# Optimization experiments

Measured on AMD Instinct MI355X. Metric: run time of the kernel, lower is better.

The kernel has to match this reference:

```python
import jax, jax.numpy as jnp
import numpy as np

TOP_K = 8
SCORE_FUNC = "sigmoid"
ROUTE_NORM = True
ROUTE_SCALE = 2.5


def setup_inputs() -> dict:
    key = jax.random.key(0)
    k1, k2, k3 = jax.random.split(key, 3)
    B, S, H, E = 4, 4096, 2048, 64
    hidden_states = jax.random.normal(k1, (B, S, H), dtype=jnp.float32)
    # nn.Linear default init scale ~ 1/sqrt(H); exact distribution irrelevant for correctness
    gate_w = jax.random.normal(k2, (E, H), dtype=jnp.float32) * (1.0 / np.sqrt(H))
    expert_bias = jax.random.normal(k3, (E,), dtype=jnp.float32) * 0.1
    return {"hidden_states": hidden_states, "expert_bias": expert_bias, "gate_w": gate_w}


def reference(hidden_states, expert_bias, gate_w):
    B, S, H = hidden_states.shape
    x = hidden_states.reshape(-1, H)  # [T, H]
    logits = jnp.einsum("th,eh->te", x, gate_w)  # [T, E]
    if SCORE_FUNC == "sigmoid":
        scores = jax.nn.sigmoid(logits.astype(jnp.float32))
    else:
        scores = jax.nn.softmax(logits.astype(jnp.float32), axis=-1)
    if expert_bias is not None:
        _, selected_experts = jax.lax.top_k(scores + expert_bias[None, :], TOP_K)
        top_scores = jnp.take_along_axis(scores, selected_experts, axis=1)
    else:
        top_scores, selected_experts = jax.lax.top_k(scores, TOP_K)
    if SCORE_FUNC == "sigmoid" and ROUTE_NORM:
        denom = jnp.sum(top_scores, axis=-1, keepdims=True) + 1e-20
        top_scores = top_scores / denom
    top_scores = top_scores * ROUTE_SCALE
    return top_scores, selected_experts
```

## Files before the change

### kernel.cpp

```cpp
#include <hip/hip_runtime.h>
#include <math.h>

#define T_TOTAL 16384
#define HDIM    2048
#define NEXP    64

typedef unsigned short ushort_t;
using bf16x8 = __attribute__((ext_vector_type(8))) short;
using f32x4  = __attribute__((ext_vector_type(4))) float;

__device__ __forceinline__ unsigned cvtpk_bf16(float a, float b) {
    unsigned r;
    asm("v_cvt_pk_bf16_f32 %0, %1, %2" : "=v"(r) : "v"(a), "v"(b));
    return r;
}

__device__ __forceinline__ void split8(const float4 a, const float4 b,
                                       bf16x8& h, bf16x8& m, bf16x8& l) {
    const float f[8] = {a.x, a.y, a.z, a.w, b.x, b.y, b.z, b.w};
    union { unsigned u[4]; bf16x8 v; } H, M, L;
#pragma unroll
    for (int d = 0; d < 4; ++d) {
        const float f0 = f[2*d], f1 = f[2*d+1];
        const unsigned ph = cvtpk_bf16(f0, f1);
        const float r0 = f0 - __uint_as_float(ph << 16);
        const float r1 = f1 - __uint_as_float(ph & 0xFFFF0000u);
        const unsigned pm = cvtpk_bf16(r0, r1);
        const float s0 = r0 - __uint_as_float(pm << 16);
        const float s1 = r1 - __uint_as_float(pm & 0xFFFF0000u);
        H.u[d] = ph;
        M.u[d] = pm;
        L.u[d] = cvtpk_bf16(s0, s1);
    }
    h = H.v; m = M.v; l = L.v;
}

__device__ __forceinline__ void load_lds16(const void* g, void* lds) {
    __builtin_amdgcn_global_load_lds(
        (const __attribute__((address_space(1))) unsigned int*)g,
        (__attribute__((address_space(3))) unsigned int*)lds, 16, 0, 0);
}

__device__ __forceinline__ int xswz(int row) {
    return ((row & 7) << 1) | ((row >> 3) & 1);
}

__global__ __launch_bounds__(256)
void convert_w_kernel(const float* __restrict__ w, ushort_t* __restrict__ wt)
{
    const int idx = blockIdx.x * 256 + threadIdx.x;
    const int e   = idx >> 8;
    const int c8  = idx & 255;
    const int kc  = c8 >> 3;
    const int c   = c8 & 7;

    const float* src = w + (size_t)e * HDIM + kc * 64 + c * 8;
    const float4 v0 = *(const float4*)(src);
    const float4 v1 = *(const float4*)(src + 4);
    bf16x8 H, M, L;
    split8(v0, v1, H, M, L);

    const int slot = c ^ (e & 7);
    bf16x8* base = (bf16x8*)wt;
    base[((size_t)(kc * 3 + 0) * 64 + e) * 8 + slot] = H;
    base[((size_t)(kc * 3 + 1) * 64 + e) * 8 + slot] = M;
    base[((size_t)(kc * 3 + 2) * 64 + e) * 8 + slot] = L;
}

__global__ __launch_bounds__(256, 2)
void router_fused(const float* __restrict__ x,
                  const ushort_t* __restrict__ wt,
                  const float* __restrict__ bias,
                  float* __restrict__ out_scores,
                  float* __restrict__ out_idx)
{
    __shared__ __align__(16) float    Xs[2][32 * 64];
    __shared__ __align__(16) ushort_t Ws[2][3 * 64 * 64];

    const int tid  = threadIdx.x;
    const int wv   = tid >> 6;
    const int lane = tid & 63;
    const int t0   = blockIdx.x * 32;
    const int a    = wv >> 1;
    const int b    = wv & 1;
    const int lr   = lane & 15;
    const int lg   = lane >> 4;

    const float bv = bias[lane];

    const int xrow0 = wv * 8 + (lane >> 4);
    const int xrow1 = xrow0 + 4;
    const float* xsrc0 = x + (size_t)(t0 + xrow0) * HDIM + ((lane & 15) ^ xswz(xrow0)) * 4;
    const float* xsrc1 = x + (size_t)(t0 + xrow1) * HDIM + ((lane & 15) ^ xswz(xrow1)) * 4;

    const ushort_t* wsrc = wt + (size_t)(wv * 6) * 512 + lane * 8;

    f32x4 acc[8];
#pragma unroll
    for (int i = 0; i < 8; ++i) {
        f32x4 z = {0.0f, 0.0f, 0.0f, 0.0f};
        acc[i] = z;
    }

    const int rowX = a * 16 + lr;
    const int swzX = xswz(rowX);

    auto stage = [&](int kc, int bi) {
        const int ko = kc * 64;
        load_lds16(xsrc0 + ko, &Xs[bi][(wv * 2 + 0) * 256]);
        load_lds16(xsrc1 + ko, &Xs[bi][(wv * 2 + 1) * 256]);
        const ushort_t* wn = wsrc + (size_t)kc * 12288;
#pragma unroll
        for (int q = 0; q < 6; ++q)
            load_lds16(wn + q * 512, &Ws[bi][(wv * 6 + q) * 512]);
    };

#define COMPUTE(BI, PAR) do {                                                 \
    const float*  rb  = &Xs[BI][rowX * 64];                                   \
    const bf16x8* wbp = (const bf16x8*)&Ws[BI][0];                            \
    _Pragma("unroll")                                                         \
    for (int ks = 0; ks < 2; ++ks) {                                          \
        const int g0 = ks * 8 + lg * 2;                                       \
        const float4 c0 = *(const float4*)(rb + ((g0       ^ swzX) * 4));     \
        const float4 c1 = *(const float4*)(rb + (((g0 + 1) ^ swzX) * 4));     \
        bf16x8 Ah, Am, Al;                                                    \
        split8(c0, c1, Ah, Am, Al);                                           \
        _Pragma("unroll")                                                     \
        for (int n = 0; n < 2; ++n) {                                         \
            const int e    = b * 32 + n * 16 + lr;                            \
            const int slot = (ks * 4 + lg) ^ (e & 7);                         \
            const bf16x8 Bh = wbp[(0 * 64 + e) * 8 + slot];                   \
            const bf16x8 Bm = wbp[(1 * 64 + e) * 8 + slot];                   \
            const bf16x8 Bl = wbp[(2 * 64 + e) * 8 + slot];                   \
            f32x4 t = acc[(PAR) * 4 + ks * 2 + n];                            \
            t = __builtin_amdgcn_mfma_f32_16x16x32_bf16(Ah, Bh, t, 0, 0, 0);  \
            t = __builtin_amdgcn_mfma_f32_16x16x32_bf16(Am, Bh, t, 0, 0, 0);  \
            t = __builtin_amdgcn_mfma_f32_16x16x32_bf16(Ah, Bm, t, 0, 0, 0);  \
            t = __builtin_amdgcn_mfma_f32_16x16x32_bf16(Am, Bm, t, 0, 0, 0);  \
            t = __builtin_amdgcn_mfma_f32_16x16x32_bf16(Al, Bh, t, 0, 0, 0);  \
            t = __builtin_amdgcn_mfma_f32_16x16x32_bf16(Ah, Bl, t, 0, 0, 0);  \
            t = __builtin_amdgcn_mfma_f32_16x16x32_bf16(Al, Bm, t, 0, 0, 0);  \
            t = __builtin_amdgcn_mfma_f32_16x16x32_bf16(Am, Bl, t, 0, 0, 0);  \
            acc[(PAR) * 4 + ks * 2 + n] = t;                                  \
        }                                                                     \
    }                                                                         \
} while (0)

    stage(0, 0);
    __syncthreads();

#pragma unroll 1
    for (int j = 0; j < 16; ++j) {
        const int kc0 = j * 2;
        stage(kc0 + 1, 1);
        COMPUTE(0, 0);
        __syncthreads();
        if (kc0 + 2 < 32) stage(kc0 + 2, 0);
        COMPUTE(1, 1);
        __syncthreads();
    }
#undef COMPUTE

    float* ov = &Xs[0][0];
#pragma unroll
    for (int n = 0; n < 2; ++n) {
        const f32x4 s = (acc[0 * 4 + 0 * 2 + n] + acc[0 * 4 + 1 * 2 + n])
                      + (acc[1 * 4 + 0 * 2 + n] + acc[1 * 4 + 1 * 2 + n]);
#pragma unroll
        for (int r = 0; r < 4; ++r) {
            const int t = a * 16 + lg * 4 + r;
            const int e = b * 32 + n * 16 + lr;
            ov[t * 64 + e] = s[r];
        }
    }
    __syncthreads();

#pragma unroll 1
    for (int i = 0; i < 8; ++i) {
        const int t = wv * 8 + i;
        const float logit = ov[t * 64 + lane];

        const float score = 1.0f / (1.0f + expf(-logit));
        float key = score + bv;

        float myscore = 0.0f;
        int   myidx   = 0;
        float denom   = 0.0f;

#pragma unroll
        for (int r = 0; r < 8; ++r) {
            float bk = key;
#pragma unroll
            for (int off = 32; off > 0; off >>= 1)
                bk = fmaxf(bk, __shfl_xor(bk, off));
            const unsigned long long msk = __ballot(key == bk);
            const int bi = __ffsll((long long)msk) - 1;
            const float wsc = __shfl(score, bi);
            denom += wsc;
            if (lane == r)  { myscore = wsc; myidx = bi; }
            if (lane == bi) key = -__builtin_inff();
        }

        const float factor = 2.5f / (denom + 1e-20f);
        if (lane < 8) {
            out_scores[(size_t)(t0 + t) * 8 + lane] = myscore * factor;
            out_idx  [(size_t)(t0 + t) * 8 + lane] = (float)myidx;
        }
    }
}

__global__ void router_gemm_naive(const float* __restrict__ x,
                                  const float* __restrict__ w,
                                  float* __restrict__ partial)
{
    const int t = blockIdx.x;
    const int e = threadIdx.x;
    const float* xp = x + (size_t)t * HDIM;
    const float* wp = w + (size_t)e * HDIM;
    float s = 0.0f;
    for (int k = 0; k < HDIM; ++k) s = fmaf(xp[k], wp[k], s);
    partial[(size_t)t * NEXP + e] = s;
}

__global__ __launch_bounds__(256)
void router_topk_naive(const float* __restrict__ partial,
                       const float* __restrict__ bias,
                       float* __restrict__ out_scores,
                       float* __restrict__ out_idx)
{
    const int token = blockIdx.x * 4 + (threadIdx.x >> 6);
    const int lane  = threadIdx.x & 63;
    const float logit = partial[(size_t)token * NEXP + lane];
    const float score = 1.0f / (1.0f + expf(-logit));
    float key = score + bias[lane];
    float myscore = 0.0f; int myidx = 0; float denom = 0.0f;
#pragma unroll
    for (int r = 0; r < 8; ++r) {
        float bk = key;
#pragma unroll
        for (int off = 32; off > 0; off >>= 1)
            bk = fmaxf(bk, __shfl_xor(bk, off));
        const unsigned long long msk = __ballot(key == bk);
        const int bi = __ffsll((long long)msk) - 1;
        const float wsc = __shfl(score, bi);
        denom += wsc;
        if (lane == r)  { myscore = wsc; myidx = bi; }
        if (lane == bi) key = -__builtin_inff();
    }
    const float factor = 2.5f / (denom + 1e-20f);
    if (lane < 8) {
        out_scores[(size_t)token * 8 + lane] = myscore * factor;
        out_idx  [(size_t)token * 8 + lane] = (float)myidx;
    }
}

extern "C" void kernel_launch(void* const* d_in, const int* in_sizes, int n_in,
                              void* d_out, int out_size, void* d_ws, size_t ws_size,
                              hipStream_t stream)
{
    const float* x    = (const float*)d_in[0];
    const float* bias = (const float*)d_in[1];
    const float* w    = (const float*)d_in[2];

    float* out = (float*)d_out;

    const size_t wtBytes = (size_t)3 * NEXP * HDIM * sizeof(ushort_t);

    if (ws_size >= wtBytes) {
        ushort_t* wt = (ushort_t*)d_ws;
        convert_w_kernel<<<dim3(64), dim3(256), 0, stream>>>(w, wt);
        router_fused<<<dim3(T_TOTAL / 32), dim3(256), 0, stream>>>(
            x, wt, bias, out, out + (size_t)T_TOTAL * 8);
    } else {
        float* partial = (float*)d_ws;
        router_gemm_naive<<<dim3(T_TOTAL), dim3(64), 0, stream>>>(x, w, partial);
        router_topk_naive<<<dim3(T_TOTAL / 4), dim3(256), 0, stream>>>(
            partial, bias, out, out + (size_t)T_TOTAL * 8);
    }
}
```

Before: 229.3 us.

## Read pre-packed weight fragments directly from global, drop weight LDS staging

The weight-conversion kernel now writes bf16 hi/mid/lo fragments in the exact per-lane MFMA register order, so the router kernel loads B operands straight from global/L2 instead of staging the 48KB of weights per block through LDS. The block grows to 512 threads (8 waves, each owning a 16x16 output tile), and LDS shrinks to just the X tile. This cuts LDS traffic and footprint to allow higher occupancy, but B loads now hit the cache each iteration with latency not hidden by double-buffering.

Result: no change. 232.0 us (+1.2%).

```diff
diff --git a/kernel.cpp b/kernel.cpp
--- a/kernel.cpp
+++ b/kernel.cpp
@@ -48,56 +48,56 @@
 __global__ __launch_bounds__(256)
 void convert_w_kernel(const float* __restrict__ w, ushort_t* __restrict__ wt)
 {
-    const int idx = blockIdx.x * 256 + threadIdx.x;
-    const int e   = idx >> 8;
-    const int c8  = idx & 255;
-    const int kc  = c8 >> 3;
-    const int c   = c8 & 7;
-
-    const float* src = w + (size_t)e * HDIM + kc * 64 + c * 8;
+    const int f  = blockIdx.x * 256 + threadIdx.x;
+    const int kc = f >> 9;
+    const int ks = (f >> 8) & 1;
+    const int nt = (f >> 6) & 3;
+    const int l  = f & 63;
+    const int e  = nt * 16 + (l & 15);
+    const int k  = kc * 64 + ks * 32 + (l >> 4) * 8;
+
+    const float* src = w + (size_t)e * HDIM + k;
     const float4 v0 = *(const float4*)(src);
     const float4 v1 = *(const float4*)(src + 4);
     bf16x8 H, M, L;
     split8(v0, v1, H, M, L);
 
-    const int slot = c ^ (e & 7);
-    bf16x8* base = (bf16x8*)wt;
-    base[((size_t)(kc * 3 + 0) * 64 + e) * 8 + slot] = H;
-    base[((size_t)(kc * 3 + 1) * 64 + e) * 8 + slot] = M;
-    base[((size_t)(kc * 3 + 2) * 64 + e) * 8 + slot] = L;
-}
-
-__global__ __launch_bounds__(256, 2)
+    bf16x8* out = (bf16x8*)wt;
+    const int base = (f >> 6) * 3;
+    out[(size_t)(base + 0) * 64 + l] = H;
+    out[(size_t)(base + 1) * 64 + l] = M;
+    out[(size_t)(base + 2) * 64 + l] = L;
+}
+
+__global__ __launch_bounds__(512, 4)
 void router_fused(const float* __restrict__ x,
                   const ushort_t* __restrict__ wt,
                   const float* __restrict__ bias,
                   float* __restrict__ out_scores,
                   float* __restrict__ out_idx)
 {
-    __shared__ __align__(16) float    Xs[2][32 * 64];
-    __shared__ __align__(16) ushort_t Ws[2][3 * 64 * 64];
+    __shared__ __align__(16) float Xs[2][32 * 64];
 
     const int tid  = threadIdx.x;
     const int wv   = tid >> 6;
     const int lane = tid & 63;
     const int t0   = blockIdx.x * 32;
-    const int a    = wv >> 1;
-    const int b    = wv & 1;
+    const int a    = wv >> 2;
+    const int b    = wv & 3;
     const int lr   = lane & 15;
     const int lg   = lane >> 4;
 
     const float bv = bias[lane];
 
-    const int xrow0 = wv * 8 + (lane >> 4);
-    const int xrow1 = xrow0 + 4;
-    const float* xsrc0 = x + (size_t)(t0 + xrow0) * HDIM + ((lane & 15) ^ xswz(xrow0)) * 4;
-    const float* xsrc1 = x + (size_t)(t0 + xrow1) * HDIM + ((lane & 15) ^ xswz(xrow1)) * 4;
-
-    const ushort_t* wsrc = wt + (size_t)(wv * 6) * 512 + lane * 8;
-
-    f32x4 acc[8];
-#pragma unroll
-    for (int i = 0; i < 8; ++i) {
+    const int xrow = wv * 4 + (lane >> 4);
+    const float* xsrc = x + (size_t)(t0 + xrow) * HDIM
+                          + ((lane & 15) ^ xswz(xrow)) * 4;
+
+    const ushort_t* wbp = wt + (size_t)b * 1536 + (size_t)lane * 8;
+
+    f32x4 acc[4];
+#pragma unroll
+    for (int i = 0; i < 4; ++i) {
         f32x4 z = {0.0f, 0.0f, 0.0f, 0.0f};
         acc[i] = z;
     }
@@ -106,18 +106,11 @@
     const int swzX = xswz(rowX);
 
     auto stage = [&](int kc, int bi) {
-        const int ko = kc * 64;
-        load_lds16(xsrc0 + ko, &Xs[bi][(wv * 2 + 0) * 256]);
-        load_lds16(xsrc1 + ko, &Xs[bi][(wv * 2 + 1) * 256]);
-        const ushort_t* wn = wsrc + (size_t)kc * 12288;
-#pragma unroll
-        for (int q = 0; q < 6; ++q)
-            load_lds16(wn + q * 512, &Ws[bi][(wv * 6 + q) * 512]);
+        load_lds16(xsrc + kc * 64, &Xs[bi][(wv * 4) * 64]);
     };
 
-#define COMPUTE(BI, PAR) do {                                                 \
-    const float*  rb  = &Xs[BI][rowX * 64];                                   \
-    const bf16x8* wbp = (const bf16x8*)&Ws[BI][0];                            \
+#define COMPUTE(BI, PAR, KC) do {                                             \
+    const float* rb = &Xs[BI][rowX * 64];                                     \
     _Pragma("unroll")                                                         \
     for (int ks = 0; ks < 2; ++ks) {                                          \
         const int g0 = ks * 8 + lg * 2;                                       \
@@ -125,24 +118,20 @@
         const float4 c1 = *(const float4*)(rb + (((g0 + 1) ^ swzX) * 4));     \
         bf16x8 Ah, Am, Al;                                                    \
         split8(c0, c1, Ah, Am, Al);                                           \
-        _Pragma("unroll")                                                     \
-        for (int n = 0; n < 2; ++n) {                                         \
-            const int e    = b * 32 + n * 16 + lr;                            \
-            const int slot = (ks * 4 + lg) ^ (e & 7);                         \
-            const bf16x8 Bh = wbp[(0 * 64 + e) * 8 + slot];                   \
-            const bf16x8 Bm = wbp[(1 * 64 + e) * 8 + slot];                   \
-            const bf16x8 Bl = wbp[(2 * 64 + e) * 8 + slot];                   \
-            f32x4 t = acc[(PAR) * 4 + ks * 2 + n];                            \
-            t = __builtin_amdgcn_mfma_f32_16x16x32_bf16(Ah, Bh, t, 0, 0, 0);  \
-            t = __builtin_amdgcn_mfma_f32_16x16x32_bf16(Am, Bh, t, 0, 0, 0);  \
-            t = __builtin_amdgcn_mfma_f32_16x16x32_bf16(Ah, Bm, t, 0, 0, 0);  \
-            t = __builtin_amdgcn_mfma_f32_16x16x32_bf16(Am, Bm, t, 0, 0, 0);  \
-            t = __builtin_amdgcn_mfma_f32_16x16x32_bf16(Al, Bh, t, 0, 0, 0);  \
-            t = __builtin_amdgcn_mfma_f32_16x16x32_bf16(Ah, Bl, t, 0, 0, 0);  \
-            t = __builtin_amdgcn_mfma_f32_16x16x32_bf16(Al, Bm, t, 0, 0, 0);  \
-            t = __builtin_amdgcn_mfma_f32_16x16x32_bf16(Am, Bl, t, 0, 0, 0);  \
-            acc[(PAR) * 4 + ks * 2 + n] = t;                                  \
-        }                                                                     \
+        const ushort_t* bb = wbp + (size_t)(KC) * 12288 + ks * 6144;          \
+        const bf16x8 Bh = *(const bf16x8*)(bb);                               \
+        const bf16x8 Bm = *(const bf16x8*)(bb + 512);                         \
+        const bf16x8 Bl = *(const bf16x8*)(bb + 1024);                        \
+        f32x4 t = acc[(PAR) * 2 + ks];                                        \
+        t = __builtin_amdgcn_mfma_f32_16x16x32_bf16(Ah, Bh, t, 0, 0, 0);      \
+        t = __builtin_amdgcn_mfma_f32_16x16x32_bf16(Am, Bh, t, 0, 0, 0);      \
+        t = __builtin_amdgcn_mfma_f32_16x16x32_bf16(Ah, Bm, t, 0, 0, 0);      \
+        t = __builtin_amdgcn_mfma_f32_16x16x32_bf16(Am, Bm, t, 0, 0, 0);      \
+        t = __builtin_amdgcn_mfma_f32_16x16x32_bf16(Al, Bh, t, 0, 0, 0);      \
+        t = __builtin_amdgcn_mfma_f32_16x16x32_bf16(Ah, Bl, t, 0, 0, 0);      \
+        t = __builtin_amdgcn_mfma_f32_16x16x32_bf16(Al, Bm, t, 0, 0, 0);      \
+        t = __builtin_amdgcn_mfma_f32_16x16x32_bf16(Am, Bl, t, 0, 0, 0);      \
+        acc[(PAR) * 2 + ks] = t;                                              \
     }                                                                         \
 } while (0)
 
@@ -153,31 +142,24 @@
     for (int j = 0; j < 16; ++j) {
         const int kc0 = j * 2;
         stage(kc0 + 1, 1);
-        COMPUTE(0, 0);
+        COMPUTE(0, 0, kc0);
         __syncthreads();
         if (kc0 + 2 < 32) stage(kc0 + 2, 0);
-        COMPUTE(1, 1);
+        COMPUTE(1, 1, kc0 + 1);
         __syncthreads();
     }
 #undef COMPUTE
 
     float* ov = &Xs[0][0];
-#pragma unroll
-    for (int n = 0; n < 2; ++n) {
-        const f32x4 s = (acc[0 * 4 + 0 * 2 + n] + acc[0 * 4 + 1 * 2 + n])
-                      + (acc[1 * 4 + 0 * 2 + n] + acc[1 * 4 + 1 * 2 + n]);
-#pragma unroll
-        for (int r = 0; r < 4; ++r) {
-            const int t = a * 16 + lg * 4 + r;
-            const int e = b * 32 + n * 16 + lr;
-            ov[t * 64 + e] = s[r];
-        }
-    }
+    const f32x4 s = (acc[0] + acc[1]) + (acc[2] + acc[3]);
+#pragma unroll
+    for (int r = 0; r < 4; ++r)
+        ov[(a * 16 + lg * 4 + r) * 64 + b * 16 + lr] = s[r];
     __syncthreads();
 
 #pragma unroll 1
-    for (int i = 0; i < 8; ++i) {
-        const int t = wv * 8 + i;
+    for (int i = 0; i < 4; ++i) {
+        const int t = wv * 4 + i;
         const float logit = ov[t * 64 + lane];
 
         const float score = 1.0f / (1.0f + expf(-logit));
@@ -269,7 +251,7 @@
     if (ws_size >= wtBytes) {
         ushort_t* wt = (ushort_t*)d_ws;
         convert_w_kernel<<<dim3(64), dim3(256), 0, stream>>>(w, wt);
-        router_fused<<<dim3(T_TOTAL / 32), dim3(256), 0, stream>>>(
+        router_fused<<<dim3(T_TOTAL / 32), dim3(512), 0, stream>>>(
             x, wt, bias, out, out + (size_t)T_TOTAL * 8);
     } else {
         float* partial = (float*)d_ws;
```
